# Performance work log

Measured on AMD Instinct MI355X. Metric: run time of the kernel, lower is better.

Reference implementation:

```python
import jax, jax.numpy as jnp
import numpy as np

B, E, NH = 32, 4096, 32
D = E // NH            # head_dim = 128
MAX_TOKENS = 2048
MAX_POS = 1536         # next_pos values in [0, MAX_POS); max pinned so max_k is static


def setup_inputs() -> dict:
    key = jax.random.key(0)
    k0, k1, k2, k3, k4, k5 = jax.random.split(key, 6)
    x = jax.random.normal(k0, (B, 1, E), jnp.float32)
    next_pos = jax.random.randint(k1, (B,), 0, MAX_POS, jnp.int32)
    next_pos = next_pos.at[0].set(MAX_POS - 1)  # pin max so sliced cache length is fixed
    scale = 0.02
    Wq = jax.random.normal(k2, (D, E), jnp.float32) * scale
    Wk = jax.random.normal(k3, (D, E), jnp.float32) * scale
    Wv = jax.random.normal(k4, (D, E), jnp.float32) * scale
    kv_cache = jax.random.normal(k5, (2, B, MAX_TOKENS, D), jnp.float32) * scale
    return {"x": x, "Wq": Wq, "Wk": Wk, "Wv": Wv, "kv_cache": kv_cache, "next_pos": next_pos}


def reference(x, Wq, Wk, Wv, kv_cache, next_pos):
    # x: (B, 1, E); torch Linear(y = x @ W.T)
    q = jnp.einsum('bse,de->bsd', x, Wq)  # (B,1,D)
    k = jnp.einsum('bse,de->bsd', x, Wk)
    v = jnp.einsum('bse,de->bsd', x, Wv)

    # scatter the new step into the cache at each sequence's next_pos
    bidx = jnp.arange(x.shape[0])
    kv = kv_cache.at[0, bidx, next_pos].set(k[:, 0])
    kv = kv.at[1, bidx, next_pos].set(v[:, 0])

    next_pos_new = next_pos + 1
    max_k = int(jax.device_get(jnp.max(next_pos_new)))  # static given pinned next_pos

    k_cache = kv[0, :, :max_k]  # (B, max_k, D)
    v_cache = kv[1, :, :max_k]

    scores = jnp.einsum('bsd,btd->bst', q, k_cache) * (D ** -0.5)  # (B,1,max_k)
    # Faithful to torch: (max_k,max_k) tril mask broadcasts scores to (B,max_k,max_k)
    tril = jnp.tril(jnp.ones((max_k, max_k), dtype=bool))
    masked = jnp.where(tril[None], scores, -jnp.inf)  # (B, max_k, max_k)
    attn = jax.nn.softmax(masked, axis=-1)
    out = attn @ v_cache  # (B, max_k, D)
    return out
```

## Files before the change

kernel.cpp:

```cpp
#include <hip/hip_runtime.h>
#include <math.h>

#define CHUNK 32
#define MAXNC 128

__global__ void proj_kernel(const float* __restrict__ x,
                            const float* __restrict__ Wq,
                            const float* __restrict__ Wk,
                            const float* __restrict__ Wv,
                            float* __restrict__ qkv,
                            int B, int E, int D)
{
    int d = blockIdx.x;
    int b = blockIdx.y;
    int lane = threadIdx.x;
    const float* xrow = x + (size_t)b * E;
    size_t woff = (size_t)d * E;
    float aq = 0.f, ak = 0.f, av = 0.f;
    for (int i = lane * 4; i < E; i += 64 * 4) {
        float4 x4 = *(const float4*)(xrow + i);
        float4 q4 = *(const float4*)(Wq + woff + i);
        float4 k4 = *(const float4*)(Wk + woff + i);
        float4 v4 = *(const float4*)(Wv + woff + i);
        aq += x4.x*q4.x + x4.y*q4.y + x4.z*q4.z + x4.w*q4.w;
        ak += x4.x*k4.x + x4.y*k4.y + x4.z*k4.z + x4.w*k4.w;
        av += x4.x*v4.x + x4.y*v4.y + x4.z*v4.z + x4.w*v4.w;
    }
    #pragma unroll
    for (int off = 32; off >= 1; off >>= 1) {
        aq += __shfl_xor(aq, off, 64);
        ak += __shfl_xor(ak, off, 64);
        av += __shfl_xor(av, off, 64);
    }
    if (lane == 0) {
        qkv[(size_t)b * D + d] = aq;
        qkv[((size_t)B + b) * D + d] = ak;
        qkv[((size_t)2 * B + b) * D + d] = av;
    }
}

__global__ void score_chunk_kernel(const float* __restrict__ kv,
                                   const float* __restrict__ qkv,
                                   const int* __restrict__ next_pos,
                                   float* __restrict__ s_out,
                                   float* __restrict__ m_out,
                                   float* __restrict__ l_out,
                                   float* __restrict__ acc_out,
                                   int B, int D, int T, int MT, int NC, float scale)
{
    int c = blockIdx.x;
    int b = blockIdx.y;
    int tid = threadIdx.x;
    int wave = tid >> 6;
    int lane = tid & 63;
    int l16 = lane & 15;
    int g16 = lane >> 4;

    __shared__ float s_sh[CHUNK];
    __shared__ float w_sh[CHUNK];
    __shared__ float part[8][128];

    int np = next_pos[b];
    int t0 = c * CHUNK;
    const float* q    = qkv + (size_t)b * D;
    const float* knew = qkv + ((size_t)B + b) * D;
    const float* kbase = kv + (size_t)b * MT * D;
    const float4* vnew4 = (const float4*)(qkv + ((size_t)2 * B + b) * D);
    const float4* vbase4 = (const float4*)(kv + ((size_t)B + b) * MT * D);

    float4 qa = *(const float4*)(q + l16 * 8);
    float4 qb = *(const float4*)(q + l16 * 8 + 4);

    #pragma unroll
    for (int p = 0; p < 2; ++p) {
        int j = wave * 8 + p * 4 + g16;
        int t = t0 + j;
        const float* krow = (t == np) ? knew : (kbase + (size_t)t * D);
        float4 ka = *(const float4*)(krow + l16 * 8);
        float4 kb = *(const float4*)(krow + l16 * 8 + 4);
        float ps = qa.x*ka.x + qa.y*ka.y + qa.z*ka.z + qa.w*ka.w
                 + qb.x*kb.x + qb.y*kb.y + qb.z*kb.z + qb.w*kb.w;
        ps += __shfl_xor(ps, 1, 64);
        ps += __shfl_xor(ps, 2, 64);
        ps += __shfl_xor(ps, 4, 64);
        ps += __shfl_xor(ps, 8, 64);
        if (l16 == 0) {
            float sv = (t < T) ? ps * scale : -1e30f;
            s_sh[j] = sv;
            if (t < T) s_out[(size_t)b * T + t] = sv;
        }
    }
    __syncthreads();

    if (wave == 0) {
        float sv = s_sh[lane & 31];
        float m = sv;
        #pragma unroll
        for (int off = 16; off >= 1; off >>= 1)
            m = fmaxf(m, __shfl_xor(m, off, 64));
        float w = __expf(sv - m);
        w_sh[lane & 31] = w;
        float l = w;
        #pragma unroll
        for (int off = 16; off >= 1; off >>= 1)
            l += __shfl_xor(l, off, 64);
        if (lane == 0) {
            m_out[(size_t)b * NC + c] = m;
            l_out[(size_t)b * NC + c] = l;
        }
    }
    __syncthreads();

    int rg = tid >> 5;
    int d4 = tid & 31;
    float4 a4 = make_float4(0.f, 0.f, 0.f, 0.f);
    #pragma unroll
    for (int p = 0; p < 4; ++p) {
        int j = rg * 4 + p;
        int t = t0 + j;
        float4 vv = (t == np) ? vnew4[d4] : vbase4[(size_t)t * 32 + d4];
        float w = w_sh[j];
        a4.x += w * vv.x; a4.y += w * vv.y; a4.z += w * vv.z; a4.w += w * vv.w;
    }
    ((float4*)&part[rg][d4 * 4])[0] = a4;
    __syncthreads();
    if (tid < 128) {
        float s = 0.f;
        #pragma unroll
        for (int r = 0; r < 8; ++r) s += part[r][tid];
        acc_out[((size_t)b * NC + c) * D + tid] = s;
    }
}

__global__ void scan_kernel(const float* __restrict__ m_in,
                            const float* __restrict__ l_in,
                            const float* __restrict__ acc_in,
                            float* __restrict__ Mc_out,
                            float* __restrict__ carryL_out,
                            float* __restrict__ carryA_out,
                            int B, int D, int NC)
{
    int b = blockIdx.x;
    int tid = threadIdx.x;

    extern __shared__ float sh[];
    float* accs = sh;
    float* m_l  = sh + (size_t)NC * 128;
    float* l_l  = m_l + NC;

    const float4* asrc = (const float4*)(acc_in + (size_t)b * NC * D);
    float4* adst = (float4*)accs;
    for (int i = tid; i < NC * 32; i += 128)
        adst[i] = asrc[i];
    if (tid < NC) {
        m_l[tid] = m_in[(size_t)b * NC + tid];
        l_l[tid] = l_in[(size_t)b * NC + tid];
    }
    __syncthreads();

    float M = -1e30f, A = 0.f, L = 0.f;
    float* caout = carryA_out + (size_t)b * NC * D + tid;
    for (int c = 0; c < NC; ++c) {
        float mc = m_l[c];
        float Mn = fmaxf(M, mc);
        float e_old = __expf(M - Mn);
        float Ac = A * e_old;
        caout[(size_t)c * D] = Ac;
        if (tid == 0) {
            Mc_out[(size_t)b * NC + c] = Mn;
            carryL_out[(size_t)b * NC + c] = L * e_old;
        }
        float e_c = __expf(mc - Mn);
        A = Ac + e_c * accs[c * 128 + tid];
        L = L * e_old + e_c * l_l[c];
        M = Mn;
    }
}

__global__ void out_kernel(const float* __restrict__ kv,
                           const float* __restrict__ qkv,
                           const int* __restrict__ next_pos,
                           const float* __restrict__ s_in,
                           const float* __restrict__ Mc_in,
                           const float* __restrict__ carryL_in,
                           const float* __restrict__ carryA_in,
                           float* __restrict__ out,
                           int B, int D, int T, int MT, int NC)
{
    int c = blockIdx.x;
    int b = blockIdx.y;
    int tid = threadIdx.x;

    __shared__ float vs[CHUNK * 128];
    __shared__ float w_sh[CHUNK];
    __shared__ float rl_sh[CHUNK];

    int np = next_pos[b];
    int t0 = c * CHUNK;
    float M = Mc_in[(size_t)b * NC + c];

    const float4* vnew4 = (const float4*)(qkv + ((size_t)2 * B + b) * D);
    const float4* vbase4 = (const float4*)(kv + ((size_t)B + b) * MT * D);

    float A = 0.f;
    if (tid < 128) {
        A = carryA_in[((size_t)b * NC + c) * D + tid];
        if (tid < CHUNK) {
            int t = t0 + tid;
            w_sh[tid] = (t < T) ? __expf(s_in[(size_t)b * T + t] - M) : 0.f;
        }
    } else {
        int t2 = tid - 128;
        #pragma unroll
        for (int r = 0; r < 8; ++r) {
            int i4 = t2 + r * 128;
            int j = i4 >> 5;
            int t = t0 + j;
            float4 vv = (t == np) ? vnew4[i4 & 31]
                                  : vbase4[(size_t)t * 32 + (i4 & 31)];
            ((float4*)vs)[i4] = vv;
        }
    }
    __syncthreads();

    if (tid < CHUNK) {
        float L = carryL_in[(size_t)b * NC + c];
        for (int r = 0; r <= tid; ++r)
            L += w_sh[r];
        rl_sh[tid] = 1.0f / L;
    }
    __syncthreads();

    if (tid < 128) {
        float* orow = out + ((size_t)b * T + t0) * (size_t)D + tid;
        #pragma unroll
        for (int j = 0; j < CHUNK; ++j) {
            int t = t0 + j;
            if (t >= T) break;
            A += w_sh[j] * vs[j * 128 + tid];
            orow[(size_t)j * D] = A * rl_sh[j];
        }
    }
}

extern "C" void kernel_launch(void* const* d_in, const int* in_sizes, int n_in,
                              void* d_out, int out_size, void* d_ws, size_t ws_size,
                              hipStream_t stream) {
    const float* x        = (const float*)d_in[0];
    const float* Wq       = (const float*)d_in[1];
    const float* Wk       = (const float*)d_in[2];
    const float* Wv       = (const float*)d_in[3];
    const float* kv       = (const float*)d_in[4];
    const int*   next_pos = (const int*)d_in[5];
    float* out = (float*)d_out;

    const int B  = in_sizes[5];
    const int E  = in_sizes[0] / B;
    const int D  = in_sizes[1] / E;
    const int T  = out_size / (B * D);
    const int MT = in_sizes[4] / (2 * B * D);
    const int NC = (T + CHUNK - 1) / CHUNK;

    float* ws     = (float*)d_ws;
    float* qkv    = ws;
    float* s      = qkv + (size_t)3 * B * D;
    float* m      = s + (size_t)B * T;
    float* l      = m + (size_t)B * NC;
    float* acc    = l + (size_t)B * NC;
    float* Mc     = acc + (size_t)B * NC * D;
    float* carryL = Mc + (size_t)B * NC;
    float* carryA = carryL + (size_t)B * NC;

    const float scale = 1.0f / sqrtf((float)D);

    proj_kernel<<<dim3(D, B), 64, 0, stream>>>(x, Wq, Wk, Wv, qkv, B, E, D);
    score_chunk_kernel<<<dim3(NC, B), 256, 0, stream>>>(kv, qkv, next_pos,
                                                        s, m, l, acc,
                                                        B, D, T, MT, NC, scale);
    size_t scan_lds = ((size_t)NC * 128 + 2 * NC) * sizeof(float);
    scan_kernel<<<dim3(B), 128, scan_lds, stream>>>(m, l, acc, Mc, carryL, carryA,
                                                    B, D, NC);
    out_kernel<<<dim3(NC, B), 256, 0, stream>>>(kv, qkv, next_pos,
                                                s, Mc, carryL, carryA, out,
                                                B, D, T, MT, NC);
}
```

Before: 135.2 us.

## Hoist V loads, store chunk softmax weights, use shuffle scan for prefix sums

Score kernel now issues K and V global loads up front so the V fetch overlaps the score/softmax phase, and stores the per-chunk exponentiated weights instead of raw scores. The out kernel reuses those weights with a rescale factor instead of recomputing exp, loads V across all 256 threads, and replaces the serial per-thread prefix sum with a wavefront shuffle scan. Smaller tweaks unroll the projection loop and prefetch the next accumulator in the scan kernel. Holding the V loads in registers earlier raises register pressure.

```diff
diff --git a/kernel.cpp b/kernel.cpp
--- a/kernel.cpp
+++ b/kernel.cpp
@@ -2,7 +2,6 @@
 #include <math.h>
 
 #define CHUNK 32
-#define MAXNC 128
 
 __global__ void proj_kernel(const float* __restrict__ x,
                             const float* __restrict__ Wq,
@@ -17,7 +16,10 @@
     const float* xrow = x + (size_t)b * E;
     size_t woff = (size_t)d * E;
     float aq = 0.f, ak = 0.f, av = 0.f;
-    for (int i = lane * 4; i < E; i += 64 * 4) {
+    int iters = E >> 8;
+    #pragma unroll 4
+    for (int it = 0; it < iters; ++it) {
+        int i = lane * 4 + it * 256;
         float4 x4 = *(const float4*)(xrow + i);
         float4 q4 = *(const float4*)(Wq + woff + i);
         float4 k4 = *(const float4*)(Wk + woff + i);
@@ -42,7 +44,7 @@
 __global__ void score_chunk_kernel(const float* __restrict__ kv,
                                    const float* __restrict__ qkv,
                                    const int* __restrict__ next_pos,
-                                   float* __restrict__ s_out,
+                                   float* __restrict__ w_out,
                                    float* __restrict__ m_out,
                                    float* __restrict__ l_out,
                                    float* __restrict__ acc_out,
@@ -71,24 +73,43 @@
     float4 qa = *(const float4*)(q + l16 * 8);
     float4 qb = *(const float4*)(q + l16 * 8 + 4);
 
-    #pragma unroll
-    for (int p = 0; p < 2; ++p) {
-        int j = wave * 8 + p * 4 + g16;
-        int t = t0 + j;
-        const float* krow = (t == np) ? knew : (kbase + (size_t)t * D);
-        float4 ka = *(const float4*)(krow + l16 * 8);
-        float4 kb = *(const float4*)(krow + l16 * 8 + 4);
-        float ps = qa.x*ka.x + qa.y*ka.y + qa.z*ka.z + qa.w*ka.w
-                 + qb.x*kb.x + qb.y*kb.y + qb.z*kb.z + qb.w*kb.w;
+    int j0 = wave * 8 + g16;
+    int j1 = wave * 8 + 4 + g16;
+    int ta = t0 + j0, tb = t0 + j1;
+    const float* krowa = (ta == np) ? knew : (kbase + (size_t)ta * D);
+    const float* krowb = (tb == np) ? knew : (kbase + (size_t)tb * D);
+    float4 ka0 = *(const float4*)(krowa + l16 * 8);
+    float4 kb0 = *(const float4*)(krowa + l16 * 8 + 4);
+    float4 ka1 = *(const float4*)(krowb + l16 * 8);
+    float4 kb1 = *(const float4*)(krowb + l16 * 8 + 4);
+
+    int rg = tid >> 5;
+    int d4 = tid & 31;
+    float4 v0, v1, v2, v3;
+    {
+        int t;
+        t = t0 + rg * 4 + 0; v0 = (t == np) ? vnew4[d4] : vbase4[(size_t)t * 32 + d4];
+        t = t0 + rg * 4 + 1; v1 = (t == np) ? vnew4[d4] : vbase4[(size_t)t * 32 + d4];
+        t = t0 + rg * 4 + 2; v2 = (t == np) ? vnew4[d4] : vbase4[(size_t)t * 32 + d4];
+        t = t0 + rg * 4 + 3; v3 = (t == np) ? vnew4[d4] : vbase4[(size_t)t * 32 + d4];
+    }
+
+    {
+        float ps = qa.x*ka0.x + qa.y*ka0.y + qa.z*ka0.z + qa.w*ka0.w
+                 + qb.x*kb0.x + qb.y*kb0.y + qb.z*kb0.z + qb.w*kb0.w;
         ps += __shfl_xor(ps, 1, 64);
         ps += __shfl_xor(ps, 2, 64);
         ps += __shfl_xor(ps, 4, 64);
         ps += __shfl_xor(ps, 8, 64);
-        if (l16 == 0) {
-            float sv = (t < T) ? ps * scale : -1e30f;
-            s_sh[j] = sv;
-            if (t < T) s_out[(size_t)b * T + t] = sv;
-        }
+        if (l16 == 0) s_sh[j0] = (ta < T) ? ps * scale : -1e30f;
+
+        float pt = qa.x*ka1.x + qa.y*ka1.y + qa.z*ka1.z + qa.w*ka1.w
+                 + qb.x*kb1.x + qb.y*kb1.y + qb.z*kb1.z + qb.w*kb1.w;
+        pt += __shfl_xor(pt, 1, 64);
+        pt += __shfl_xor(pt, 2, 64);
+        pt += __shfl_xor(pt, 4, 64);
+        pt += __shfl_xor(pt, 8, 64);
+        if (l16 == 0) s_sh[j1] = (tb < T) ? pt * scale : -1e30f;
     }
     __syncthreads();
 
@@ -104,6 +125,8 @@
         #pragma unroll
         for (int off = 16; off >= 1; off >>= 1)
             l += __shfl_xor(l, off, 64);
+        if (lane < 32 && t0 + lane < T)
+            w_out[(size_t)b * T + t0 + lane] = w;
         if (lane == 0) {
             m_out[(size_t)b * NC + c] = m;
             l_out[(size_t)b * NC + c] = l;
@@ -111,18 +134,16 @@
     }
     __syncthreads();
 
-    int rg = tid >> 5;
-    int d4 = tid & 31;
-    float4 a4 = make_float4(0.f, 0.f, 0.f, 0.f);
-    #pragma unroll
-    for (int p = 0; p < 4; ++p) {
-        int j = rg * 4 + p;
-        int t = t0 + j;
-        float4 vv = (t == np) ? vnew4[d4] : vbase4[(size_t)t * 32 + d4];
-        float w = w_sh[j];
-        a4.x += w * vv.x; a4.y += w * vv.y; a4.z += w * vv.z; a4.w += w * vv.w;
-    }
-    ((float4*)&part[rg][d4 * 4])[0] = a4;
+    {
+        float w0 = w_sh[rg * 4 + 0], w1 = w_sh[rg * 4 + 1];
+        float w2 = w_sh[rg * 4 + 2], w3 = w_sh[rg * 4 + 3];
+        float4 a4;
+        a4.x = w0*v0.x + w1*v1.x + w2*v2.x + w3*v3.x;
+        a4.y = w0*v0.y + w1*v1.y + w2*v2.y + w3*v3.y;
+        a4.z = w0*v0.z + w1*v1.z + w2*v2.z + w3*v3.z;
+        a4.w = w0*v0.w + w1*v1.w + w2*v2.w + w3*v3.w;
+        ((float4*)&part[rg][d4 * 4])[0] = a4;
+    }
     __syncthreads();
     if (tid < 128) {
         float s = 0.f;
@@ -160,7 +181,10 @@
 
     float M = -1e30f, A = 0.f, L = 0.f;
     float* caout = carryA_out + (size_t)b * NC * D + tid;
+    float a_next = accs[tid];
     for (int c = 0; c < NC; ++c) {
+        float a_c = a_next;
+        if (c + 1 < NC) a_next = accs[(c + 1) * 128 + tid];
         float mc = m_l[c];
         float Mn = fmaxf(M, mc);
         float e_old = __expf(M - Mn);
@@ -171,7 +195,7 @@
             carryL_out[(size_t)b * NC + c] = L * e_old;
         }
         float e_c = __expf(mc - Mn);
-        A = Ac + e_c * accs[c * 128 + tid];
+        A = Ac + e_c * a_c;
         L = L * e_old + e_c * l_l[c];
         M = Mn;
     }
@@ -180,7 +204,8 @@
 __global__ void out_kernel(const float* __restrict__ kv,
                            const float* __restrict__ qkv,
                            const int* __restrict__ next_pos,
-                           const float* __restrict__ s_in,
+                           const float* __restrict__ w_in,
+                           const float* __restrict__ m_in,
                            const float* __restrict__ Mc_in,
                            const float* __restrict__ carryL_in,
                            const float* __restrict__ carryA_in,
@@ -197,36 +222,46 @@
 
     int np = next_pos[b];
     int t0 = c * CHUNK;
-    float M = Mc_in[(size_t)b * NC + c];
 
     const float4* vnew4 = (const float4*)(qkv + ((size_t)2 * B + b) * D);
     const float4* vbase4 = (const float4*)(kv + ((size_t)B + b) * MT * D);
 
+    float4 sv0, sv1, sv2, sv3;
+    {
+        int i4, t;
+        i4 = tid;       t = t0 + (i4 >> 5);
+        sv0 = (t == np) ? vnew4[i4 & 31] : vbase4[(size_t)t * 32 + (i4 & 31)];
+        i4 = tid + 256; t = t0 + (i4 >> 5);
+        sv1 = (t == np) ? vnew4[i4 & 31] : vbase4[(size_t)t * 32 + (i4 & 31)];
+        i4 = tid + 512; t = t0 + (i4 >> 5);
+        sv2 = (t == np) ? vnew4[i4 & 31] : vbase4[(size_t)t * 32 + (i4 & 31)];
+        i4 = tid + 768; t = t0 + (i4 >> 5);
+        sv3 = (t == np) ? vnew4[i4 & 31] : vbase4[(size_t)t * 32 + (i4 & 31)];
+    }
     float A = 0.f;
-    if (tid < 128) {
+    if (tid < 128)
         A = carryA_in[((size_t)b * NC + c) * D + tid];
-        if (tid < CHUNK) {
-            int t = t0 + tid;
-            w_sh[tid] = (t < T) ? __expf(s_in[(size_t)b * T + t] - M) : 0.f;
+    float wv = 0.f;
+    float f = 0.f;
+    if (tid < CHUNK) {
+        int t = t0 + tid;
+        f = __expf(m_in[(size_t)b * NC + c] - Mc_in[(size_t)b * NC + c]);
+        wv = (t < T) ? w_in[(size_t)b * T + t] * f : 0.f;
+    }
+
+    ((float4*)vs)[tid]       = sv0;
+    ((float4*)vs)[tid + 256] = sv1;
+    ((float4*)vs)[tid + 512] = sv2;
+    ((float4*)vs)[tid + 768] = sv3;
+    if (tid < CHUNK) {
+        w_sh[tid] = wv;
+        float xacc = wv;
+        #pragma unroll
+        for (int off = 1; off < 32; off <<= 1) {
+            float n = __shfl_up(xacc, off, 64);
+            if (tid >= off) xacc += n;
         }
-    } else {
-        int t2 = tid - 128;
-        #pragma unroll
-        for (int r = 0; r < 8; ++r) {
-            int i4 = t2 + r * 128;
-            int j = i4 >> 5;
-            int t = t0 + j;
-            float4 vv = (t == np) ? vnew4[i4 & 31]
-                                  : vbase4[(size_t)t * 32 + (i4 & 31)];
-            ((float4*)vs)[i4] = vv;
-        }
-    }
-    __syncthreads();
-
-    if (tid < CHUNK) {
-        float L = carryL_in[(size_t)b * NC + c];
-        for (int r = 0; r <= tid; ++r)
-            L += w_sh[r];
+        float L = carryL_in[(size_t)b * NC + c] + xacc;
         rl_sh[tid] = 1.0f / L;
     }
     __syncthreads();
@@ -263,8 +298,8 @@
 
     float* ws     = (float*)d_ws;
     float* qkv    = ws;
-    float* s      = qkv + (size_t)3 * B * D;
-    float* m      = s + (size_t)B * T;
+    float* w      = qkv + (size_t)3 * B * D;
+    float* m      = w + (size_t)B * T;
     float* l      = m + (size_t)B * NC;
     float* acc    = l + (size_t)B * NC;
     float* Mc     = acc + (size_t)B * NC * D;
@@ -275,12 +310,12 @@
 
     proj_kernel<<<dim3(D, B), 64, 0, stream>>>(x, Wq, Wk, Wv, qkv, B, E, D);
     score_chunk_kernel<<<dim3(NC, B), 256, 0, stream>>>(kv, qkv, next_pos,
-                                                        s, m, l, acc,
+                                                        w, m, l, acc,
                                                         B, D, T, MT, NC, scale);
     size_t scan_lds = ((size_t)NC * 128 + 2 * NC) * sizeof(float);
     scan_kernel<<<dim3(B), 128, scan_lds, stream>>>(m, l, acc, Mc, carryL, carryA,
                                                     B, D, NC);
     out_kernel<<<dim3(NC, B), 256, 0, stream>>>(kv, qkv, next_pos,
-                                                s, Mc, carryL, carryA, out,
+                                                w, m, Mc, carryL, carryA, out,
                                                 B, D, T, MT, NC);
 }
```

Measured after the change: 135.3 us, median of 2. Within noise of the previous version (+0.1%).
